# Kernel tuning notes

Measured on AMD Instinct MI355X. Metric: run time of the kernel, lower is better.

## Reference

```python
import jax, jax.numpy as jnp
import numpy as np

N_NODES = 50000
N_EDGES = 800000
IN_C, HID_C, OUT_C = 128, 128, 64


def setup_inputs() -> dict:
    key = jax.random.key(0)
    k1, k2, k3, k4, k5 = jax.random.split(key, 5)
    x = jax.random.normal(k1, (N_NODES, IN_C), dtype=jnp.float32)
    edge_index = jax.random.randint(k2, (2, N_EDGES), 0, N_NODES, dtype=jnp.int64)
    # Glorot-style init for GCN weights, zero bias (PyG GCNConv defaults)
    s1 = (6.0 / (IN_C + HID_C)) ** 0.5
    s2 = (6.0 / (HID_C + OUT_C)) ** 0.5
    W1 = jax.random.uniform(k3, (IN_C, HID_C), jnp.float32, -s1, s1)
    W2 = jax.random.uniform(k4, (HID_C, OUT_C), jnp.float32, -s2, s2)
    b1 = jnp.zeros((HID_C,), jnp.float32)
    b2 = jnp.zeros((OUT_C,), jnp.float32)
    return {"x": x, "edge_index": edge_index, "W1": W1, "b1": b1, "W2": W2, "b2": b2}


def _gcn_conv(x, src, dst, W, b, n_nodes):
    # PyG GCNConv: add self-loops, symmetric normalization, linear transform,
    # scatter-add aggregation from src (row) to dst (col), then bias.
    h = x @ W  # [N, out]
    loops = jnp.arange(n_nodes, dtype=src.dtype)
    src_f = jnp.concatenate([src, loops])
    dst_f = jnp.concatenate([dst, loops])
    deg = jax.ops.segment_sum(jnp.ones_like(dst_f, dtype=h.dtype), dst_f,
                              num_segments=n_nodes)  # in-degree incl. self-loop
    dinv = jnp.where(deg > 0, jax.lax.rsqrt(deg), 0.0)
    norm = dinv[src_f] * dinv[dst_f]  # [E + N]
    msgs = h[src_f] * norm[:, None]   # gather + scale
    out = jax.ops.segment_sum(msgs, dst_f, num_segments=n_nodes)  # scatter-add
    return out + b


def reference(x, edge_index, W1, b1, W2, b2):
    src, dst = edge_index[0], edge_index[1]
    n = x.shape[0]
    h = jax.nn.relu(_gcn_conv(x, src, dst, W1, b1, n))
    return _gcn_conv(h, src, dst, W2, b2, n)
```

## Files before the change

### kernel.cpp

```cpp
#include <hip/hip_runtime.h>
#include <hip/hip_bf16.h>
#include <hip/hip_fp16.h>


#define NBUCK 800
#define CHUNK 2048
#define STASH 2048

__global__ __launch_bounds__(256) void presort_k(const int* __restrict__ src,
                                                 const int* __restrict__ dst,
                                                 unsigned* __restrict__ rec2,
                                                 int* __restrict__ hist2,
                                                 int* __restrict__ runstart2,
                                                 int E) {
    __shared__ int lh[NBUCK], lscan[NBUCK], cur[NBUCK];
    __shared__ int sred[256];
    __shared__ unsigned srec[CHUNK];
    int t = threadIdx.x;
    int lo = blockIdx.x * CHUNK, hi = min(E, lo + CHUNK);

    for (int i = t; i < NBUCK; i += 256) lh[i] = 0;
    __syncthreads();
    for (int e = lo + t; e < hi; e += 256)
        atomicAdd(&lh[dst[e] >> 6], 1);
    __syncthreads();

    int base = t * 4;
    int v[4];
    int s = 0;
#pragma unroll
    for (int i = 0; i < 4; ++i) {
        int idx = base + i;
        int c = (idx < NBUCK) ? lh[idx] : 0;
        v[i] = c; s += c;
    }
    sred[t] = s;
    __syncthreads();
#pragma unroll
    for (int off = 1; off < 256; off <<= 1) {
        int x = 0;
        if (t >= off) x = sred[t - off];
        __syncthreads();
        sred[t] += x;
        __syncthreads();
    }
    int run = sred[t] - s;
#pragma unroll
    for (int i = 0; i < 4; ++i) {
        int idx = base + i;
        if (idx < NBUCK) { lscan[idx] = run; cur[idx] = run; }
        run += v[i];
    }
    __syncthreads();

    for (int e = lo + t; e < hi; e += 256) {
        int d = dst[e];
        int p = atomicAdd(&cur[d >> 6], 1);
        srec[p] = (unsigned)(src[e] & 0xffff) | ((unsigned)d << 16);
    }
    __syncthreads();

    int n = hi - lo;
    for (int j = t; j < n; j += 256) rec2[lo + j] = srec[j];
    int hbase = blockIdx.x * NBUCK;
    for (int b = t; b < NBUCK; b += 256) {
        hist2[hbase + b] = lh[b];
        runstart2[hbase + b] = lscan[b];
    }
}

__global__ __launch_bounds__(256) void coltot_k(const int* __restrict__ hist2,
                                                int* __restrict__ btot, int BCNT) {
    __shared__ int sred[256];
    int b = blockIdx.x, t = threadIdx.x;
    int s = 0;
    for (int i = t; i < BCNT; i += 256) s += hist2[i * NBUCK + b];
    sred[t] = s;
    __syncthreads();
#pragma unroll
    for (int off = 128; off > 0; off >>= 1) {
        if (t < off) sred[t] += sred[t + off];
        __syncthreads();
    }
    if (t == 0) btot[b] = sred[0];
}

__global__ __launch_bounds__(256) void scan800_k(const int* __restrict__ btot,
                                                 int* __restrict__ bucketBase,
                                                 int* __restrict__ offsets,
                                                 int N, int E) {
    __shared__ int sred[256];
    int t = threadIdx.x;
    int base = t * 4;
    int v[4];
    int s = 0;
#pragma unroll
    for (int i = 0; i < 4; ++i) {
        int idx = base + i;
        int c = (idx < NBUCK) ? btot[idx] : 0;
        v[i] = c; s += c;
    }
    sred[t] = s;
    __syncthreads();
#pragma unroll
    for (int off = 1; off < 256; off <<= 1) {
        int x = 0;
        if (t >= off) x = sred[t - off];
        __syncthreads();
        sred[t] += x;
        __syncthreads();
    }
    int run = sred[t] - s;
#pragma unroll
    for (int i = 0; i < 4; ++i) {
        int idx = base + i;
        if (idx < NBUCK) bucketBase[idx] = run;
        run += v[i];
    }
    if (t == 255) bucketBase[NBUCK] = run;
    if (t == 0) offsets[N] = E;
}

__global__ __launch_bounds__(256) void finish2_k(const unsigned* __restrict__ rec2,
                                                 const int* __restrict__ hist2,
                                                 const int* __restrict__ runstart2,
                                                 const int* __restrict__ bucketBase,
                                                 int* __restrict__ offsets,
                                                 float* __restrict__ dinv,
                                                 unsigned short* __restrict__ adj,
                                                 int BCNT, int N) {
    __shared__ int ncnt[64], ncur[64], nodeOff[64];
    __shared__ int stashCnt;
    __shared__ unsigned stash[STASH];
    __shared__ unsigned short adjl[STASH];
    int b = blockIdx.x, t = threadIdx.x;
    if (t < 64) { ncnt[t] = 0; ncur[t] = 0; }
    if (t == 0) stashCnt = 0;
    __syncthreads();

    for (int i = t; i < BCNT; i += 256) {
        int len = hist2[i * NBUCK + b];
        if (!len) continue;
        int gbase = i * CHUNK + runstart2[i * NBUCK + b];
        int sp = atomicAdd(&stashCnt, len);
        for (int k = 0; k < len; ++k) {
            unsigned r = rec2[gbase + k];
            atomicAdd(&ncnt[(r >> 16) & 63], 1);
            if (sp + k < STASH) stash[sp + k] = r;
        }
    }
    __syncthreads();

    if (t == 0) {
        int r = 0;
#pragma unroll
        for (int i = 0; i < 64; ++i) { nodeOff[i] = r; r += ncnt[i]; }
    }
    __syncthreads();

    int bstart = bucketBase[b];
    if (t < 64) {
        int gnode = b * 64 + t;
        if (gnode < N) {
            dinv[gnode] = rsqrtf((float)(ncnt[t] + 1));
            offsets[gnode] = bstart + nodeOff[t];
        }
    }
    __syncthreads();

    int tot = stashCnt;
    if (tot > STASH) tot = STASH;
    for (int j = t; j < tot; j += 256) {
        unsigned r = stash[j];
        int ln = (r >> 16) & 63;
        int p = atomicAdd(&ncur[ln], 1);
        adjl[nodeOff[ln] + p] = (unsigned short)(r & 0xffff);
    }
    __syncthreads();
    for (int j = t; j < tot; j += 256) adj[bstart + j] = adjl[j];
}

template <int NOUT, bool HALF_IN>
__global__ __launch_bounds__(256) void gemm_scale_k(const void* __restrict__ Xv,
                                                    const float* __restrict__ W,
                                                    const float* __restrict__ dinv,
                                                    __half* __restrict__ Hout, int M) {
    constexpr int K = 128;
    constexpr int BM = 64;
    constexpr int COLCH = NOUT / 4;
    constexpr int RG = 256 / COLCH;
    constexpr int ROWS = BM / RG;
    __shared__ float xs[BM][K];

    int t = threadIdx.x;
    int brow = blockIdx.x * BM;

    if constexpr (HALF_IN) {
        const __half* X = (const __half*)Xv;
        for (int i = t; i < BM * (K / 8); i += 256) {
            int row = i / (K / 8);
            int c8 = i % (K / 8);
            int gr = brow + row;
            float f[8] = {0.f, 0.f, 0.f, 0.f, 0.f, 0.f, 0.f, 0.f};
            if (gr < M) {
                uint4 u = *(const uint4*)(X + (size_t)gr * K + c8 * 8);
                const __half2* hp = (const __half2*)&u;
#pragma unroll
                for (int j = 0; j < 4; ++j) {
                    float2 fj = __half22float2(hp[j]);
                    f[2 * j] = fj.x;
                    f[2 * j + 1] = fj.y;
                }
            }
#pragma unroll
            for (int j = 0; j < 8; ++j) xs[row][c8 * 8 + j] = f[j];
        }
    } else {
        const float* X = (const float*)Xv;
        for (int i = t; i < BM * (K / 4); i += 256) {
            int row = i / (K / 4);
            int c4 = i % (K / 4);
            float4 v = make_float4(0.f, 0.f, 0.f, 0.f);
            int gr = brow + row;
            if (gr < M) v = *(const float4*)(X + (size_t)gr * K + c4 * 4);
            *(float4*)(&xs[row][c4 * 4]) = v;
        }
    }
    __syncthreads();

    int cc = t % COLCH;
    int rg = t / COLCH;

    float acc[ROWS][4];
#pragma unroll
    for (int r = 0; r < ROWS; ++r) {
        acc[r][0] = 0.f; acc[r][1] = 0.f; acc[r][2] = 0.f; acc[r][3] = 0.f;
    }

    for (int k4 = 0; k4 < K / 4; ++k4) {
        float4 xv[ROWS];
#pragma unroll
        for (int r = 0; r < ROWS; ++r)
            xv[r] = *(const float4*)(&xs[rg * ROWS + r][k4 * 4]);
#pragma unroll
        for (int kk = 0; kk < 4; ++kk) {
            float4 w = *(const float4*)(W + (size_t)(k4 * 4 + kk) * NOUT + cc * 4);
#pragma unroll
            for (int r = 0; r < ROWS; ++r) {
                float xvk = ((const float*)&xv[r])[kk];
                acc[r][0] += xvk * w.x;
                acc[r][1] += xvk * w.y;
                acc[r][2] += xvk * w.z;
                acc[r][3] += xvk * w.w;
            }
        }
    }

#pragma unroll
    for (int r = 0; r < ROWS; ++r) {
        int gr = brow + rg * ROWS + r;
        if (gr < M) {
            float s = dinv[gr];
            union { __half2 h[2]; uint2 u; } pk;
            pk.h[0] = __floats2half2_rn(acc[r][0] * s, acc[r][1] * s);
            pk.h[1] = __floats2half2_rn(acc[r][2] * s, acc[r][3] * s);
            *(uint2*)(Hout + (size_t)gr * NOUT + cc * 4) = pk.u;
        }
    }
}

__device__ __forceinline__ void ld_row(const __half* p, float (&f)[4]) {
    uint2 u = *(const uint2*)p;
    const __half2* hp = (const __half2*)&u;
    float2 a = __half22float2(hp[0]);
    float2 b = __half22float2(hp[1]);
    f[0] = a.x; f[1] = a.y; f[2] = b.x; f[3] = b.y;
}
__device__ __forceinline__ void ld_row(const __half* p, float (&f)[2]) {
    float2 a = __half22float2(*(const __half2*)p);
    f[0] = a.x; f[1] = a.y;
}

template <int C, bool RELU, typename TOUT>
__global__ __launch_bounds__(256) void aggregate_k(const __half* __restrict__ H,
                                                   const int* __restrict__ offsets,
                                                   const unsigned short* __restrict__ adj,
                                                   const float* __restrict__ dinv,
                                                   const float* __restrict__ bias,
                                                   TOUT* __restrict__ out, int n) {
    constexpr int V = C / 32;
    int wave = threadIdx.x >> 6;
    int lane = threadIdx.x & 63;
    int half_id = lane >> 5;
    int sub = lane & 31;
    int node = blockIdx.x * 8 + wave * 2 + half_id;
    if (node >= n) return;

    const __half* hl = H + sub * V;

    float acc[V];
    ld_row(hl + (size_t)node * C, acc);

    int e0 = offsets[node], e1 = offsets[node + 1];
    int e = e0;

    for (; e + 8 <= e1; e += 8) {
        int s[8];
#pragma unroll
        for (int j = 0; j < 8; ++j) s[j] = adj[e + j];
        float t[8][V];
#pragma unroll
        for (int j = 0; j < 8; ++j) ld_row(hl + (size_t)s[j] * C, t[j]);
#pragma unroll
        for (int v = 0; v < V; ++v)
            acc[v] += ((t[0][v] + t[1][v]) + (t[2][v] + t[3][v])) +
                      ((t[4][v] + t[5][v]) + (t[6][v] + t[7][v]));
    }
    for (; e + 2 <= e1; e += 2) {
        int s0 = adj[e], s1 = adj[e + 1];
        float t0[V], t1[V];
        ld_row(hl + (size_t)s0 * C, t0);
        ld_row(hl + (size_t)s1 * C, t1);
#pragma unroll
        for (int v = 0; v < V; ++v) acc[v] += t0[v] + t1[v];
    }
    if (e < e1) {
        float t0[V];
        ld_row(hl + (size_t)adj[e] * C, t0);
#pragma unroll
        for (int v = 0; v < V; ++v) acc[v] += t0[v];
    }

    float di = dinv[node];
    float o[V];
#pragma unroll
    for (int v = 0; v < V; ++v) {
        o[v] = acc[v] * di + bias[sub * V + v];
        if (RELU) o[v] = fmaxf(o[v], 0.f);
    }

    if constexpr (sizeof(TOUT) == 2) {
        union { __half2 h[2]; uint2 u; } pk;
        pk.h[0] = __floats2half2_rn(o[0], o[1]);
        pk.h[1] = __floats2half2_rn(o[2], o[3]);
        *(uint2*)((__half*)out + (size_t)node * C + sub * V) = pk.u;
    } else {
        *(float2*)((float*)out + (size_t)node * C + sub * V) = make_float2(o[0], o[1]);
    }
}

extern "C" void kernel_launch(void* const* d_in, const int* in_sizes, int n_in,
                              void* d_out, int out_size, void* d_ws, size_t ws_size,
                              hipStream_t stream) {
    const float* x = (const float*)d_in[0];
    const int* ei = (const int*)d_in[1];
    const float* W1 = (const float*)d_in[2];
    const float* b1 = (const float*)d_in[3];
    const float* W2 = (const float*)d_in[4];
    const float* b2 = (const float*)d_in[5];
    float* out = (float*)d_out;

    const int IN_C = 128, HID_C = 128;
    int N = in_sizes[0] / IN_C;
    int E = in_sizes[1] / 2;
    const int* src = ei;
    const int* dst = ei + E;

    int BCNT = (E + CHUNK - 1) / CHUNK;

    int NP = (N + 255) & ~255;
    int EP = (E + 255) & ~255;
    char* w = (char*)d_ws;
    int* hist2 = (int*)w;           w += (size_t)BCNT * NBUCK * 4;
    int* runstart2 = (int*)w;       w += (size_t)BCNT * NBUCK * 4;
    int* btot = (int*)w;            w += (size_t)(NBUCK + 32) * 4;
    int* bucketBase = (int*)w;      w += (size_t)(NBUCK + 32) * 4;
    int* offsets = (int*)w;         w += (size_t)(NP + 256) * 4;
    float* dinv = (float*)w;        w += (size_t)NP * 4;
    unsigned* rec2 = (unsigned*)w;  w += (size_t)(BCNT * CHUNK) * 4;
    unsigned short* adj = (unsigned short*)w; w += (size_t)EP * 2;
    __half* H1 = (__half*)w;        w += (size_t)NP * HID_C * 2;
    __half* HID = (__half*)w;       w += (size_t)NP * HID_C * 2;
    (void)ws_size; (void)n_in; (void)out_size;

    presort_k<<<BCNT, 256, 0, stream>>>(src, dst, rec2, hist2, runstart2, E);
    coltot_k<<<NBUCK, 256, 0, stream>>>(hist2, btot, BCNT);
    scan800_k<<<1, 256, 0, stream>>>(btot, bucketBase, offsets, N, E);
    finish2_k<<<NBUCK, 256, 0, stream>>>(rec2, hist2, runstart2, bucketBase,
                                         offsets, dinv, adj, BCNT, N);

    gemm_scale_k<128, false><<<(N + 63) / 64, 256, 0, stream>>>(x, W1, dinv, H1, N);
    aggregate_k<128, true, __half><<<(N + 7) / 8, 256, 0, stream>>>(
        H1, offsets, adj, dinv, b1, HID, N);

    gemm_scale_k<64, true><<<(N + 63) / 64, 256, 0, stream>>>(HID, W2, dinv, H1, N);
    aggregate_k<64, false, float><<<(N + 7) / 8, 256, 0, stream>>>(
        H1, offsets, adj, dinv, b2, out, N);
}
```

Baseline: 139.4 us.

## Replace scalar FP32 GEMM with fp16 MFMA 16x16x32 matrix-core kernel

The per-layer dense transform is rewritten to use MFMA f32_16x16x32_f16 instructions. Inputs are pre-scaled by dinv and stored as fp16 in LDS, with W transposed into padded LDS. Output tiles are staged back through LDS so global stores can be coalesced. This replaces FP32 FMA work on the vector ALUs with matrix-core throughput, at the cost of fp16 rounding of the inputs and weights before accumulation and extra per-block LDS staging of W.

```diff
diff --git a/kernel.cpp b/kernel.cpp
--- a/kernel.cpp
+++ b/kernel.cpp
@@ -6,6 +6,9 @@
 #define NBUCK 800
 #define CHUNK 2048
 #define STASH 2048
+
+typedef float f32x4 __attribute__((ext_vector_type(4)));
+typedef _Float16 f16x8 __attribute__((ext_vector_type(8)));
 
 __global__ __launch_bounds__(256) void presort_k(const int* __restrict__ src,
                                                  const int* __restrict__ dst,
@@ -181,16 +184,16 @@
 }
 
 template <int NOUT, bool HALF_IN>
-__global__ __launch_bounds__(256) void gemm_scale_k(const void* __restrict__ Xv,
-                                                    const float* __restrict__ W,
-                                                    const float* __restrict__ dinv,
-                                                    __half* __restrict__ Hout, int M) {
+__global__ __launch_bounds__(256) void gemm_mfma_k(const void* __restrict__ Xv,
+                                                   const float* __restrict__ W,
+                                                   const float* __restrict__ dinv,
+                                                   __half* __restrict__ Hout, int M) {
     constexpr int K = 128;
     constexpr int BM = 64;
-    constexpr int COLCH = NOUT / 4;
-    constexpr int RG = 256 / COLCH;
-    constexpr int ROWS = BM / RG;
-    __shared__ float xs[BM][K];
+    constexpr int LDP = K + 8;
+    constexpr int CT = NOUT / 16;
+    __shared__ _Float16 xs[BM][LDP];
+    __shared__ _Float16 wsl[NOUT][LDP];
 
     int t = threadIdx.x;
     int brow = blockIdx.x * BM;
@@ -198,74 +201,85 @@
     if constexpr (HALF_IN) {
         const __half* X = (const __half*)Xv;
         for (int i = t; i < BM * (K / 8); i += 256) {
-            int row = i / (K / 8);
-            int c8 = i % (K / 8);
+            int row = i / (K / 8), c8 = i % (K / 8);
             int gr = brow + row;
-            float f[8] = {0.f, 0.f, 0.f, 0.f, 0.f, 0.f, 0.f, 0.f};
+            union { _Float16 h[8]; uint4 u; } pk;
             if (gr < M) {
                 uint4 u = *(const uint4*)(X + (size_t)gr * K + c8 * 8);
                 const __half2* hp = (const __half2*)&u;
+                float di = dinv[gr];
 #pragma unroll
                 for (int j = 0; j < 4; ++j) {
-                    float2 fj = __half22float2(hp[j]);
-                    f[2 * j] = fj.x;
-                    f[2 * j + 1] = fj.y;
+                    float2 f = __half22float2(hp[j]);
+                    pk.h[2 * j] = (_Float16)(f.x * di);
+                    pk.h[2 * j + 1] = (_Float16)(f.y * di);
                 }
+            } else {
+                pk.u = make_uint4(0, 0, 0, 0);
             }
-#pragma unroll
-            for (int j = 0; j < 8; ++j) xs[row][c8 * 8 + j] = f[j];
+            *(uint4*)&xs[row][c8 * 8] = pk.u;
         }
     } else {
         const float* X = (const float*)Xv;
         for (int i = t; i < BM * (K / 4); i += 256) {
-            int row = i / (K / 4);
-            int c4 = i % (K / 4);
-            float4 v = make_float4(0.f, 0.f, 0.f, 0.f);
+            int row = i / (K / 4), c4 = i % (K / 4);
             int gr = brow + row;
-            if (gr < M) v = *(const float4*)(X + (size_t)gr * K + c4 * 4);
-            *(float4*)(&xs[row][c4 * 4]) = v;
+            union { _Float16 h[4]; uint2 u; } pk;
+            if (gr < M) {
+                float4 v = *(const float4*)(X + (size_t)gr * K + c4 * 4);
+                float di = dinv[gr];
+                pk.h[0] = (_Float16)(v.x * di);
+                pk.h[1] = (_Float16)(v.y * di);
+                pk.h[2] = (_Float16)(v.z * di);
+                pk.h[3] = (_Float16)(v.w * di);
+            } else {
+                pk.u = make_uint2(0, 0);
+            }
+            *(uint2*)&xs[row][c4 * 4] = pk.u;
         }
     }
-    __syncthreads();
-
-    int cc = t % COLCH;
-    int rg = t / COLCH;
-
-    float acc[ROWS][4];
-#pragma unroll
-    for (int r = 0; r < ROWS; ++r) {
-        acc[r][0] = 0.f; acc[r][1] = 0.f; acc[r][2] = 0.f; acc[r][3] = 0.f;
-    }
-
-    for (int k4 = 0; k4 < K / 4; ++k4) {
-        float4 xv[ROWS];
-#pragma unroll
-        for (int r = 0; r < ROWS; ++r)
-            xv[r] = *(const float4*)(&xs[rg * ROWS + r][k4 * 4]);
-#pragma unroll
-        for (int kk = 0; kk < 4; ++kk) {
-            float4 w = *(const float4*)(W + (size_t)(k4 * 4 + kk) * NOUT + cc * 4);
-#pragma unroll
-            for (int r = 0; r < ROWS; ++r) {
-                float xvk = ((const float*)&xv[r])[kk];
-                acc[r][0] += xvk * w.x;
-                acc[r][1] += xvk * w.y;
-                acc[r][2] += xvk * w.z;
-                acc[r][3] += xvk * w.w;
-            }
+
+    for (int i = t; i < K * (NOUT / 4); i += 256) {
+        int k = i / (NOUT / 4), c4 = i % (NOUT / 4);
+        float4 wv = *(const float4*)(W + (size_t)k * NOUT + c4 * 4);
+        wsl[c4 * 4 + 0][k] = (_Float16)wv.x;
+        wsl[c4 * 4 + 1][k] = (_Float16)wv.y;
+        wsl[c4 * 4 + 2][k] = (_Float16)wv.z;
+        wsl[c4 * 4 + 3][k] = (_Float16)wv.w;
+    }
+    __syncthreads();
+
+    int w = t >> 6, lane = t & 63;
+    int lrow = lane & 15;
+    int lko = (lane >> 4) * 8;
+
+    f32x4 acc[CT];
+#pragma unroll
+    for (int c = 0; c < CT; ++c) acc[c] = (f32x4){0.f, 0.f, 0.f, 0.f};
+
+#pragma unroll
+    for (int s = 0; s < K / 32; ++s) {
+        f16x8 a = *(const f16x8*)&xs[w * 16 + lrow][s * 32 + lko];
+#pragma unroll
+        for (int c = 0; c < CT; ++c) {
+            f16x8 b = *(const f16x8*)&wsl[c * 16 + lrow][s * 32 + lko];
+            acc[c] = __builtin_amdgcn_mfma_f32_16x16x32_f16(a, b, acc[c], 0, 0, 0);
         }
     }
 
-#pragma unroll
-    for (int r = 0; r < ROWS; ++r) {
-        int gr = brow + rg * ROWS + r;
-        if (gr < M) {
-            float s = dinv[gr];
-            union { __half2 h[2]; uint2 u; } pk;
-            pk.h[0] = __floats2half2_rn(acc[r][0] * s, acc[r][1] * s);
-            pk.h[1] = __floats2half2_rn(acc[r][2] * s, acc[r][3] * s);
-            *(uint2*)(Hout + (size_t)gr * NOUT + cc * 4) = pk.u;
-        }
+    __syncthreads();
+#pragma unroll
+    for (int c = 0; c < CT; ++c) {
+#pragma unroll
+        for (int r = 0; r < 4; ++r)
+            xs[w * 16 + (lane >> 4) * 4 + r][c * 16 + lrow] = (_Float16)acc[c][r];
+    }
+    __syncthreads();
+    for (int j = t; j < BM * (NOUT / 8); j += 256) {
+        int row = j / (NOUT / 8), c8 = j % (NOUT / 8);
+        int gr = brow + row;
+        if (gr < M)
+            *(uint4*)(Hout + (size_t)gr * NOUT + c8 * 8) = *(uint4*)&xs[row][c8 * 8];
     }
 }
 
@@ -389,11 +403,11 @@
     finish2_k<<<NBUCK, 256, 0, stream>>>(rec2, hist2, runstart2, bucketBase,
                                          offsets, dinv, adj, BCNT, N);
 
-    gemm_scale_k<128, false><<<(N + 63) / 64, 256, 0, stream>>>(x, W1, dinv, H1, N);
+    gemm_mfma_k<128, false><<<(N + 63) / 64, 256, 0, stream>>>(x, W1, dinv, H1, N);
     aggregate_k<128, true, __half><<<(N + 7) / 8, 256, 0, stream>>>(
         H1, offsets, adj, dinv, b1, HID, N);
 
-    gemm_scale_k<64, true><<<(N + 63) / 64, 256, 0, stream>>>(HID, W2, dinv, H1, N);
+    gemm_mfma_k<64, true><<<(N + 63) / 64, 256, 0, stream>>>(HID, W2, dinv, H1, N);
     aggregate_k<64, false, float><<<(N + 7) / 8, 256, 0, stream>>>(
         H1, offsets, adj, dinv, b2, out, N);
 }
```

Measured after the change: 123.6 us. -11.4%, faster.
